# Kernel optimization log

Hardware: AMD Instinct MI355X
Metric: run time of the kernel (lower is better)

The kernel has to match this reference:

```python
import jax, jax.numpy as jnp
import numpy as np
from jax import lax

H_ENC = 64
H_DEC = 128
PRED_STEPS = 30


def _run_lstm_last(x, Wih, Whh, bih, bhh):
    """Batched LSTM (batch_first), returns last hidden state. x: [N, T, I] -> [N, H]."""
    N = x.shape[0]
    H = Whh.shape[1]
    xg = jnp.einsum('nti,gi->ntg', x, Wih) + bih  # [N, T, 4H], input projection hoisted

    def step(carry, g_t):
        h, c = carry
        gates = g_t + h @ Whh.T + bhh
        i, f, g, o = jnp.split(gates, 4, axis=-1)  # torch gate order i,f,g,o
        c = jax.nn.sigmoid(f) * c + jax.nn.sigmoid(i) * jnp.tanh(g)
        h = jax.nn.sigmoid(o) * jnp.tanh(c)
        return (h, c), None

    z = jnp.zeros((N, H), x.dtype)
    (h, _), _ = lax.scan(step, (z, z), jnp.swapaxes(xg, 0, 1))
    return h


def setup_inputs() -> dict:
    key = jax.random.key(0)
    ks = jax.random.split(key, 20)
    B, T, NMAX = 2048, 50, 16
    s = 0.1
    inp = {
        'train_agent': jax.random.normal(ks[0], (B, T, 2), jnp.float32),
        'neighbour': jax.random.normal(ks[1], (B, NMAX, T, 2), jnp.float32),
        'neighbour_counts': jax.random.randint(ks[2], (B,), 0, NMAX + 1),
        # agent encoder LSTM(2 -> 64)
        'Wih_a': jax.random.normal(ks[3], (4 * H_ENC, 2), jnp.float32) * s,
        'Whh_a': jax.random.normal(ks[4], (4 * H_ENC, H_ENC), jnp.float32) * s,
        'bih_a': jax.random.normal(ks[5], (4 * H_ENC,), jnp.float32) * s,
        'bhh_a': jax.random.normal(ks[6], (4 * H_ENC,), jnp.float32) * s,
        # neighbour encoder LSTM(2 -> 64)
        'Wih_n': jax.random.normal(ks[7], (4 * H_ENC, 2), jnp.float32) * s,
        'Whh_n': jax.random.normal(ks[8], (4 * H_ENC, H_ENC), jnp.float32) * s,
        'bih_n': jax.random.normal(ks[9], (4 * H_ENC,), jnp.float32) * s,
        'bhh_n': jax.random.normal(ks[10], (4 * H_ENC,), jnp.float32) * s,
        # decoder LSTMCell(128 -> 128)
        'Wih_d': jax.random.normal(ks[11], (4 * H_DEC, H_DEC), jnp.float32) * s,
        'Whh_d': jax.random.normal(ks[12], (4 * H_DEC, H_DEC), jnp.float32) * s,
        'bih_d': jax.random.normal(ks[13], (4 * H_DEC,), jnp.float32) * s,
        'bhh_d': jax.random.normal(ks[14], (4 * H_DEC,), jnp.float32) * s,
        # embedding_pos Linear(128 -> 2)
        'Wpos': jax.random.normal(ks[15], (2, H_DEC), jnp.float32) * s,
        'bpos': jax.random.normal(ks[16], (2,), jnp.float32) * s,
    }
    return inp


def reference(train_agent, neighbour, neighbour_counts,
              Wih_a, Whh_a, bih_a, bhh_a,
              Wih_n, Whh_n, bih_n, bhh_n,
              Wih_d, Whh_d, bih_d, bhh_d,
              Wpos, bpos):
    B, NMAX, T, _ = neighbour.shape

    # agent encoder: last hidden state  [B, 64]
    agent_emb = _run_lstm_last(train_agent, Wih_a, Whh_a, bih_a, bhh_a)

    # neighbour encoder over all padded neighbour sequences  [B*NMAX, 64]
    n_enc = _run_lstm_last(neighbour.reshape(B * NMAX, T, 2),
                           Wih_n, Whh_n, bih_n, bhh_n).reshape(B, NMAX, H_ENC)
    valid = jnp.arange(NMAX)[None, :] < neighbour_counts[:, None]  # [B, NMAX]
    neg_inf = jnp.asarray(-jnp.inf, n_enc.dtype)
    n_max = jnp.max(jnp.where(valid[:, :, None], n_enc, neg_inf), axis=1)  # [B, 64]
    neigh_emb = jnp.where((neighbour_counts > 0)[:, None], n_max,
                          jnp.zeros((), n_enc.dtype))

    # decoder: LSTMCell fed its own hidden state as input, 30 steps
    h0 = jnp.concatenate([agent_emb, neigh_emb], axis=1)  # [B, 128]
    c0 = jnp.zeros_like(h0)

    def dec_step(carry, _):
        h, c = carry
        gates = h @ Wih_d.T + bih_d + h @ Whh_d.T + bhh_d  # input == hidden == h
        i, f, g, o = jnp.split(gates, 4, axis=-1)
        c_new = jax.nn.sigmoid(f) * c + jax.nn.sigmoid(i) * jnp.tanh(g)
        h_new = jax.nn.sigmoid(o) * jnp.tanh(c_new)
        pred = h_new @ Wpos.T + bpos  # [B, 2]
        return (h_new, c_new), pred

    _, preds = lax.scan(dec_step, (h0, c0), None, length=PRED_STEPS)  # [30, B, 2]
    return jnp.swapaxes(preds, 0, 1)  # [B, 30, 2]
```

## Files before the change

### kernel.cpp

```cpp
#include <hip/hip_runtime.h>
#include <stdint.h>


#define T_SEQ 50
#define PRED_STEPS 30
#define NMAX 16

typedef float v2f __attribute__((ext_vector_type(2)));
typedef float v4f __attribute__((ext_vector_type(4)));
typedef short v8s __attribute__((ext_vector_type(8)));

#define L2E 1.44269504f
#define L2E2 2.88539008f

static constexpr size_t OFF_AEMB  = 0;
static constexpr size_t OFF_NENC  = 131072;
static constexpr size_t OFF_IDX   = 2228224;
static constexpr size_t OFF_PACKA = 2490368;
static constexpr size_t OFF_PACKN = 2498560;
static constexpr size_t OFF_WDP   = 2506752;
static constexpr size_t OFF_WDB   = 2539520;

__device__ __forceinline__ float frcp(float x) { return __builtin_amdgcn_rcpf(x); }
#if __has_builtin(__builtin_amdgcn_exp2f)
__device__ __forceinline__ float fexp2(float x) { return __builtin_amdgcn_exp2f(x); }
#else
__device__ __forceinline__ float fexp2(float x) { return exp2f(x); }
#endif
__device__ __forceinline__ unsigned bf16rne(float f) {
  unsigned u = __float_as_uint(f);
  u += 0x7fff + ((u >> 16) & 1);
  return u >> 16;
}
__device__ __forceinline__ v4f mfma16(v8s a, v8s b, v4f c) {
  return __builtin_amdgcn_mfma_f32_16x16x32_bf16(a, b, c, 0, 0, 0);
}

__device__ __forceinline__ float cell_update(float iv, float fv, float gv,
                                             float ov, float& cref) {
  float ef = fexp2(-fv);
  float ei = fexp2(-iv);
  float eg = fexp2(-gv);
  float t1 = (1.f + ei) * (1.f + eg);
  float rD = frcp((1.f + ef) * t1);
  float sf = t1 * rD;
  float u  = (1.f - eg) * ((1.f + ef) * rD);
  float cn = fmaf(sf, cref, u);
  cref = cn;
  float eo = fexp2(-ov);
  float ec = fexp2(fminf(-L2E2 * cn, 60.f));
  return (1.f - ec) * frcp((1.f + eo) * (1.f + ec));
}

__device__ __forceinline__ uint4 pack8(const float* __restrict__ p, float gs) {
  float4 w0 = *(const float4*)p;
  float4 w1 = *(const float4*)(p + 4);
  uint4 o;
  o.x = bf16rne(w0.x * gs) | (bf16rne(w0.y * gs) << 16);
  o.y = bf16rne(w0.z * gs) | (bf16rne(w0.w * gs) << 16);
  o.z = bf16rne(w1.x * gs) | (bf16rne(w1.y * gs) << 16);
  o.w = bf16rne(w1.z * gs) | (bf16rne(w1.w * gs) << 16);
  return o;
}
__device__ __forceinline__ uint4 pack8sum(const float* __restrict__ pa,
                                          const float* __restrict__ pb, float gs) {
  float4 a0 = *(const float4*)pa, a1 = *(const float4*)(pa + 4);
  float4 b0 = *(const float4*)pb, b1 = *(const float4*)(pb + 4);
  uint4 o;
  o.x = bf16rne((a0.x + b0.x) * gs) | (bf16rne((a0.y + b0.y) * gs) << 16);
  o.y = bf16rne((a0.z + b0.z) * gs) | (bf16rne((a0.w + b0.w) * gs) << 16);
  o.z = bf16rne((a1.x + b1.x) * gs) | (bf16rne((a1.y + b1.y) * gs) << 16);
  o.w = bf16rne((a1.z + b1.z) * gs) | (bf16rne((a1.w + b1.w) * gs) << 16);
  return o;
}

__global__ void prep_kernel(const float* __restrict__ Whh_a, const float* __restrict__ Whh_n,
                            const float* __restrict__ Wih_d, const float* __restrict__ Whh_d,
                            const float* __restrict__ bih_d, const float* __restrict__ bhh_d,
                            uint4* __restrict__ packA, uint4* __restrict__ packN,
                            uint4* __restrict__ packD, float* __restrict__ bd,
                            int* __restrict__ idxb) {
  const int b = blockIdx.x;
  {
    const int gi = b * 256 + threadIdx.x;
    for (int i = gi; i < 32768; i += 12288) idxb[i] = -1;
    if (gi == 0) idxb[32768] = 0;
  }
  if (b < 16) {
    const int which = b >> 3;
    const float* Whh = which ? Whh_n : Whh_a;
    uint4* dst = which ? packN : packA;
    const int idx = (b & 7) * 256 + threadIdx.x;
    const int lane = idx & 63, c = idx >> 6;
    const int kh = c & 1, g = (c >> 1) & 3, w = c >> 3;
    const float gs = (g == 2) ? L2E2 : L2E;
    const int row = g * 64 + 16 * w + (lane & 15);
    const int kb = kh * 32 + (lane >> 4) * 8;
    dst[c * 64 + lane] = pack8(Whh + row * 64 + kb, gs);
  } else {
    const int idx = (b - 16) * 256 + threadIdx.x;
    const int lane = idx & 63, c = idx >> 6;
    const int kh = c & 3, i = (c >> 2) & 1, wv = c >> 3;
    const int g = wv & 3, q = wv >> 2;
    const float gs = (g == 2) ? L2E2 : L2E;
    const int ju = q * 32 + i * 16 + (lane & 15);
    const int row = g * 128 + ju;
    const int kb = kh * 32 + (lane >> 4) * 8;
    packD[c * 64 + lane] = pack8sum(Wih_d + row * 128 + kb, Whh_d + row * 128 + kb, gs);
    if (b < 18) {
      int iB = (b - 16) * 256 + threadIdx.x;
      float s = ((iB >> 7) == 2) ? L2E2 : L2E;
      bd[iB] = (bih_d[iB] + bhh_d[iB]) * s;
    }
  }
}

__global__ void compact_kernel(const int* __restrict__ cnts, int* __restrict__ idxb) {
  const int b = blockIdx.x * 256 + threadIdx.x;
  if (b >= 2048) return;
  int cnt = cnts[b];
  cnt = cnt < 0 ? 0 : (cnt > NMAX ? NMAX : cnt);
  if (cnt == 0) return;
  int pos = atomicAdd(idxb + 32768, cnt);
  for (int j = 0; j < cnt; ++j) idxb[pos + j] = b * NMAX + j;
}

__global__ __launch_bounds__(256, 4) void enc_mfma_kernel(
    const float* __restrict__ xA, const float* __restrict__ xN,
    const v8s* __restrict__ packA, const v8s* __restrict__ packN,
    const float* __restrict__ Wih_a, const float* __restrict__ bih_a, const float* __restrict__ bhh_a,
    const float* __restrict__ Wih_n, const float* __restrict__ bih_n, const float* __restrict__ bhh_n,
    const int* __restrict__ idxb,
    float* __restrict__ outA, float* __restrict__ outN) {
  __shared__ unsigned short hph[2304];
  __shared__ float xst[1600];
  __shared__ int sidx[16];
  const int tid = threadIdx.x, lane = tid & 63, wv = tid >> 6;
  const int nb = blockIdx.x;
  const bool isA = nb >= 2048;
  const int s0 = (isA ? nb - 2048 : nb) * 16;

  if (!isA && s0 >= idxb[32768]) return;

  const float* xsrc = isA ? xA : xN;
  const v8s* pk = isA ? packA : packN;
  const float* Wih = isA ? Wih_a : Wih_n;
  const float* bih = isA ? bih_a : bih_n;
  const float* bhh = isA ? bhh_a : bhh_n;
  float* outp = isA ? outA : outN;

  v8s B[4][2];
#pragma unroll
  for (int g = 0; g < 4; ++g)
#pragma unroll
    for (int kh = 0; kh < 2; ++kh)
      B[g][kh] = pk[(wv * 8 + g * 2 + kh) * 64 + lane];

  const int jc = lane & 15, qc = lane >> 4;
  float wi0[4], wi1[4], bs[4];
#pragma unroll
  for (int g = 0; g < 4; ++g) {
    const float gs = (g == 2) ? L2E2 : L2E;
    int n = g * 64 + 16 * wv + jc;
    wi0[g] = Wih[n * 2 + 0] * gs;
    wi1[g] = Wih[n * 2 + 1] * gs;
    bs[g] = (bih[n] + bhh[n]) * gs;
  }

  {
    if (tid < 16) sidx[tid] = isA ? (s0 + tid) : idxb[s0 + tid];
    for (int i = tid; i < 576; i += 256) ((unsigned*)hph)[i] = 0;
    __syncthreads();
    for (int i = tid; i < 400; i += 256) {
      int slot = i / 25, j = i - slot * 25;
      int sq = sidx[slot];
      const float4* xb = (const float4*)(xsrc + (size_t)(sq < 0 ? 0 : sq) * 100);
      ((float4*)xst)[i] = xb[j];
    }
  }
  __syncthreads();

  const int ms = lane & 15, ks = lane >> 4;
  float cst[4] = {0.f, 0.f, 0.f, 0.f};
  float h[4];

  auto enc_step = [&](int t, int rb, int wb) {
    v4f a4[4];
#pragma unroll
    for (int r = 0; r < 4; ++r) {
      v2f xv = *(const __shared__ v2f*)&xst[(qc * 4 + r) * 100 + 2 * t];
#pragma unroll
      for (int g = 0; g < 4; ++g)
        a4[g][r] = fmaf(wi1[g], xv.y, fmaf(wi0[g], xv.x, bs[g]));
    }

#pragma unroll
    for (int kh = 0; kh < 2; ++kh) {
      v8s Ahi = *(const __shared__ v8s*)&hph[rb + ms * 72 + kh * 32 + ks * 8];
#pragma unroll
      for (int g = 0; g < 4; ++g)
        a4[g] = mfma16(Ahi, B[g][kh], a4[g]);
    }

#pragma unroll
    for (int r = 0; r < 4; ++r) {
      h[r] = cell_update(a4[0][r], a4[1][r], a4[2][r], a4[3][r], cst[r]);
      hph[wb + (qc * 4 + r) * 72 + 16 * wv + jc] =
          (unsigned short)bf16rne(h[r]);
    }
    __syncthreads();
  };

  for (int t2 = 0; t2 < T_SEQ; t2 += 2) {
    enc_step(t2 + 0, 0, 1152);
    enc_step(t2 + 1, 1152, 0);
  }

#pragma unroll
  for (int r = 0; r < 4; ++r) {
    int sq = sidx[qc * 4 + r];
    if (sq >= 0)
      outp[(size_t)sq * 64 + 16 * wv + jc] = h[r];
  }
}

__global__ __launch_bounds__(512, 2) void dec_mfma_kernel(
    const v8s* __restrict__ pkd, const float* __restrict__ bd,
    const float* __restrict__ aemb, const float* __restrict__ nenc,
    const int* __restrict__ cnts, const float* __restrict__ Wpos,
    const float* __restrict__ bpos, float* __restrict__ out) {
  __shared__ unsigned short hph[2][2176];
  __shared__ float pall[3840];
  const int tid = threadIdx.x, lane = tid & 63, wv = tid >> 6;
  const int jc = lane & 15, qc = lane >> 4;
  const int s0 = blockIdx.x * 8;

  v8s B[4][4];
  float bs[4];
#pragma unroll
  for (int g = 0; g < 4; ++g) {
#pragma unroll
    for (int kh = 0; kh < 4; ++kh)
      B[g][kh] = pkd[(((wv >> 1) * 4 + g) * 8 + (wv & 1) * 4 + kh) * 64 + lane];
    bs[g] = bd[g * 128 + wv * 16 + jc];
  }
  const float wp0 = Wpos[wv * 16 + jc];
  const float wp1 = Wpos[128 + wv * 16 + jc];
  const float bp0 = bpos[0], bp1 = bpos[1];

  for (int i = tid; i < 2176; i += 512) ((unsigned*)hph)[i] = 0;
  __syncthreads();

  for (int i = tid; i < 1024; i += 512) {
    int row = i >> 7, unit = i & 127;
    float v;
    if (unit < 64) {
      v = aemb[(size_t)(s0 + row) * 64 + unit];
    } else {
      int cnt = cnts[s0 + row];
      float m = -1e30f;
#pragma unroll
    for (int n = 0; n < NMAX; ++n) {
        float val = nenc[((size_t)((s0 + row) * NMAX + n)) * 64 + (unit - 64)];
        m = (n < cnt) ? fmaxf(m, val) : m;
      }
      v = (cnt > 0) ? m : 0.f;
    }
    hph[0][row * 136 + unit] = (unsigned short)bf16rne(v);
  }
  float cst[4] = {0.f, 0.f, 0.f, 0.f};
  __syncthreads();

  for (int t = 0; t < PRED_STEPS; ++t) {
    const int rb = t & 1, wb = rb ^ 1;
    v4f acc[4];
#pragma unroll
    for (int g = 0; g < 4; ++g)
      acc[g] = (v4f){bs[g], bs[g], bs[g], bs[g]};
#pragma unroll
    for (int kh = 0; kh < 4; ++kh) {
      v8s Ahi = *(const __shared__ v8s*)&hph[rb][jc * 136 + kh * 32 + qc * 8];
#pragma unroll
      for (int g = 0; g < 4; ++g)
        acc[g] = mfma16(Ahi, B[g][kh], acc[g]);
    }

    float hr[4];
#pragma unroll
    for (int r = 0; r < 4; ++r)
      hr[r] = cell_update(acc[0][r], acc[1][r], acc[2][r], acc[3][r], cst[r]);

    if (qc < 2) {
#pragma unroll
      for (int r = 0; r < 4; ++r)
        hph[wb][(qc * 4 + r) * 136 + wv * 16 + jc] =
            (unsigned short)bf16rne(hr[r]);
    }

    float pr0[4], pr1[4];
#pragma unroll
    for (int r = 0; r < 4; ++r) { pr0[r] = hr[r] * wp0; pr1[r] = hr[r] * wp1; }
#pragma unroll
    for (int off = 1; off < 16; off <<= 1) {
#pragma unroll
      for (int r = 0; r < 4; ++r) {
        pr0[r] += __shfl_xor(pr0[r], off, 64);
        pr1[r] += __shfl_xor(pr1[r], off, 64);
      }
    }
    if (jc == 0 && qc < 2) {
#pragma unroll
      for (int r = 0; r < 4; ++r) {
        int s = qc * 4 + r;
        pall[t * 128 + wv * 16 + s * 2 + 0] = pr0[r];
        pall[t * 128 + wv * 16 + s * 2 + 1] = pr1[r];
      }
    }
    __syncthreads();
  }

  if (tid < 480) {
    int s = tid / 60, r60 = tid - s * 60;
    int t = r60 >> 1, c = r60 & 1;
    float a = c ? bp1 : bp0;
#pragma unroll
    for (int w = 0; w < 8; ++w)
      a += pall[t * 128 + w * 16 + s * 2 + c];
    out[(size_t)(s0 + s) * 60 + r60] = a;
  }
}

extern "C" void kernel_launch(void* const* d_in, const int* in_sizes, int n_in,
                              void* d_out, int out_size, void* d_ws, size_t ws_size,
                              hipStream_t stream) {
  (void)in_sizes; (void)n_in; (void)out_size; (void)ws_size;
  const float* xA    = (const float*)d_in[0];
  const float* xN    = (const float*)d_in[1];
  const int*   cnts  = (const int*)d_in[2];
  const float* Wih_a = (const float*)d_in[3];
  const float* Whh_a = (const float*)d_in[4];
  const float* bih_a = (const float*)d_in[5];
  const float* bhh_a = (const float*)d_in[6];
  const float* Wih_n = (const float*)d_in[7];
  const float* Whh_n = (const float*)d_in[8];
  const float* bih_n = (const float*)d_in[9];
  const float* bhh_n = (const float*)d_in[10];
  const float* Wih_d = (const float*)d_in[11];
  const float* Whh_d = (const float*)d_in[12];
  const float* bih_d = (const float*)d_in[13];
  const float* bhh_d = (const float*)d_in[14];
  const float* Wpos  = (const float*)d_in[15];
  const float* bpos  = (const float*)d_in[16];
  float* out = (float*)d_out;
  float* wsf = (float*)d_ws;
  int* idxb = (int*)(wsf + OFF_IDX);

  prep_kernel<<<48, 256, 0, stream>>>(Whh_a, Whh_n, Wih_d, Whh_d, bih_d, bhh_d,
                                      (uint4*)(wsf + OFF_PACKA),
                                      (uint4*)(wsf + OFF_PACKN),
                                      (uint4*)(wsf + OFF_WDP), wsf + OFF_WDB,
                                      idxb);
  compact_kernel<<<8, 256, 0, stream>>>(cnts, idxb);
  enc_mfma_kernel<<<2176, 256, 0, stream>>>(
      xA, xN,
      (const v8s*)(wsf + OFF_PACKA), (const v8s*)(wsf + OFF_PACKN),
      Wih_a, bih_a, bhh_a, Wih_n, bih_n, bhh_n, idxb,
      wsf + OFF_AEMB, wsf + OFF_NENC);
  dec_mfma_kernel<<<256, 512, 0, stream>>>(
      (const v8s*)(wsf + OFF_WDP), wsf + OFF_WDB,
      wsf + OFF_AEMB, wsf + OFF_NENC, cnts,
      Wpos, bpos, out);
}
```

Measured before the change: 226.9 us.

## Fold neighbour compaction into prep kernel via deterministic scan; raise encoder occupancy

Replaces the separate atomic-based compaction kernel with an extra block in the prep kernel that clamps counts, does a block-wide prefix scan, and writes the compacted neighbour index list in order. Only the tail up to the next multiple of 16 is padded with -1, so the full 32K-entry index buffer is no longer cleared. This removes one kernel launch and the atomics and gives deterministic ordering. The encoder's launch bounds also rise from 4 to 8 blocks per CU, which may force register spills.

After: 755.9 us. +233.1%, slower.

```diff
diff --git a/kernel.cpp b/kernel.cpp
--- a/kernel.cpp
+++ b/kernel.cpp
@@ -77,14 +77,42 @@
 __global__ void prep_kernel(const float* __restrict__ Whh_a, const float* __restrict__ Whh_n,
                             const float* __restrict__ Wih_d, const float* __restrict__ Whh_d,
                             const float* __restrict__ bih_d, const float* __restrict__ bhh_d,
+                            const int* __restrict__ cnts,
                             uint4* __restrict__ packA, uint4* __restrict__ packN,
                             uint4* __restrict__ packD, float* __restrict__ bd,
                             int* __restrict__ idxb) {
   const int b = blockIdx.x;
-  {
-    const int gi = b * 256 + threadIdx.x;
-    for (int i = gi; i < 32768; i += 12288) idxb[i] = -1;
-    if (gi == 0) idxb[32768] = 0;
+  if (b == 48) {
+    __shared__ int wsum[4];
+    const int t = threadIdx.x, lane = t & 63, w = t >> 6;
+    int c[8], tot = 0;
+#pragma unroll
+    for (int j = 0; j < 8; ++j) {
+      int v = cnts[t * 8 + j];
+      c[j] = v < 0 ? 0 : (v > NMAX ? NMAX : v);
+      tot += c[j];
+    }
+    int inc = tot;
+#pragma unroll
+    for (int off = 1; off < 64; off <<= 1) {
+      int v = __shfl_up(inc, off, 64);
+      if (lane >= off) inc += v;
+    }
+    if (lane == 63) wsum[w] = inc;
+    __syncthreads();
+    int wbase = 0;
+    for (int k = 0; k < w; ++k) wbase += wsum[k];
+    int pos = wbase + inc - tot;
+#pragma unroll
+    for (int j = 0; j < 8; ++j)
+      for (int k = 0; k < c[j]; ++k) idxb[pos++] = (t * 8 + j) * NMAX + k;
+    if (t == 0) {
+      int Nv = wsum[0] + wsum[1] + wsum[2] + wsum[3];
+      idxb[32768] = Nv;
+      int end = (Nv + 15) & ~15;
+      for (int i = Nv; i < end; ++i) idxb[i] = -1;
+    }
+    return;
   }
   if (b < 16) {
     const int which = b >> 3;
@@ -115,17 +143,7 @@
   }
 }
 
-__global__ void compact_kernel(const int* __restrict__ cnts, int* __restrict__ idxb) {
-  const int b = blockIdx.x * 256 + threadIdx.x;
-  if (b >= 2048) return;
-  int cnt = cnts[b];
-  cnt = cnt < 0 ? 0 : (cnt > NMAX ? NMAX : cnt);
-  if (cnt == 0) return;
-  int pos = atomicAdd(idxb + 32768, cnt);
-  for (int j = 0; j < cnt; ++j) idxb[pos + j] = b * NMAX + j;
-}
-
-__global__ __launch_bounds__(256, 4) void enc_mfma_kernel(
+__global__ __launch_bounds__(256, 8) void enc_mfma_kernel(
     const float* __restrict__ xA, const float* __restrict__ xN,
     const v8s* __restrict__ packA, const v8s* __restrict__ packN,
     const float* __restrict__ Wih_a, const float* __restrict__ bih_a, const float* __restrict__ bhh_a,
@@ -355,12 +373,12 @@
   float* wsf = (float*)d_ws;
   int* idxb = (int*)(wsf + OFF_IDX);
 
-  prep_kernel<<<48, 256, 0, stream>>>(Whh_a, Whh_n, Wih_d, Whh_d, bih_d, bhh_d,
+  prep_kernel<<<49, 256, 0, stream>>>(Whh_a, Whh_n, Wih_d, Whh_d, bih_d, bhh_d,
+                                      cnts,
                                       (uint4*)(wsf + OFF_PACKA),
                                       (uint4*)(wsf + OFF_PACKN),
                                       (uint4*)(wsf + OFF_WDP), wsf + OFF_WDB,
                                       idxb);
-  compact_kernel<<<8, 256, 0, stream>>>(cnts, idxb);
   enc_mfma_kernel<<<2176, 256, 0, stream>>>(
       xA, xN,
       (const v8s*)(wsf + OFF_PACKA), (const v8s*)(wsf + OFF_PACKN),
```
